# Kernel tuning notes

Hardware: AMD Instinct MI355X
Metric: run time of the kernel (lower is better)

Reference implementation:

```python
import jax, jax.numpy as jnp
import numpy as np
from jax import lax

B, N, C, H = 8, 1024, 384, 6
D = C // H
SCALE = D ** -0.5
EPS = 1e-5


def setup_inputs() -> dict:
    key = jax.random.key(0)
    ks = jax.random.split(key, 10)
    s = 0.02
    return {
        "x": jax.random.normal(ks[0], (B, N, C), jnp.float32),
        "w_qkv": jax.random.normal(ks[1], (3 * C, C), jnp.float32) * s,
        "w_proj": jax.random.normal(ks[2], (C, C), jnp.float32) * s,
        "b_proj": jax.random.normal(ks[3], (C,), jnp.float32) * s,
        "w_kq": jax.random.normal(ks[4], (H, 1, 3, 3), jnp.float32) * 0.1,   # depthwise (groups=H)
        "b_kq": jax.random.normal(ks[5], (H,), jnp.float32) * 0.1,
        "w_head": jax.random.normal(ks[6], (H, H, 1, 1), jnp.float32) * 0.1,  # 1x1 head-mixing conv
        "b_head": jax.random.normal(ks[7], (H,), jnp.float32) * 0.1,
        "gn_w": jnp.ones((H,), jnp.float32),
        "gn_b": jnp.zeros((H,), jnp.float32),
    }


def reference(x, w_qkv, w_proj, b_proj, w_kq, b_kq, w_head, b_head, gn_w, gn_b):
    # qkv projection (torch Linear: y = x @ W.T)
    qkv = (x @ w_qkv.T).reshape(B, N, 3, H, D).transpose(2, 0, 3, 1, 4)  # [3,B,H,N,D]
    q, k, v = qkv[0], qkv[1], qkv[2]

    # attention logits [B,H,N,N]
    logits = jnp.einsum("bhnd,bhmd->bhnm", q, k) * SCALE

    # depthwise (groups=H) 3x3 conv over the NxN logit map
    logits = lax.conv_general_dilated(
        logits, w_kq, window_strides=(1, 1), padding=((1, 1), (1, 1)),
        dimension_numbers=("NCHW", "OIHW", "NCHW"), feature_group_count=H,
    ) + b_kq[None, :, None, None]

    attn = jax.nn.softmax(logits, axis=-1)

    # 1x1 conv mixing heads
    attn = jnp.einsum("oh,bhnm->bonm", w_head[:, :, 0, 0], attn) + b_head[None, :, None, None]

    # GroupNorm(num_groups=H, channels=H): per (b, head) stats over NxN
    mean = attn.mean(axis=(2, 3), keepdims=True)
    var = ((attn - mean) ** 2).mean(axis=(2, 3), keepdims=True)
    attn = (attn - mean) * lax.rsqrt(var + EPS)
    attn = attn * gn_w[None, :, None, None] + gn_b[None, :, None, None]

    out = jnp.einsum("bhnm,bhmd->bhnd", attn, v)
    out = out.transpose(0, 2, 1, 3).reshape(B, N, C)
    return out @ w_proj.T + b_proj
```

## Files before the change

### kernel.cpp

```cpp
#include <hip/hip_runtime.h>

typedef unsigned short u16;
typedef __attribute__((ext_vector_type(8))) short short8;
typedef __attribute__((ext_vector_type(4))) float f32x4;

#define MFMA(a, b, c) __builtin_amdgcn_mfma_f32_16x16x32_bf16((a), (b), (c), 0, 0, 0)

__device__ inline float bf2f(u16 u) {
  union { unsigned int i; float f; } w; w.i = ((unsigned int)u) << 16; return w.f;
}
__device__ inline u16 f2bf(float x) {
  union { float f; unsigned int i; } u; u.f = x;
  unsigned int r = u.i + 0x7fffu + ((u.i >> 16) & 1u);
  return (u16)(r >> 16);
}
__device__ inline unsigned int pk2(float a, float b) {
  return (unsigned int)f2bf(a) | ((unsigned int)f2bf(b) << 16);
}
__device__ inline void unpack8(uint4 v, float* f) {
  union { unsigned int i; float g; } c;
  c.i = v.x << 16;          f[0] = c.g;
  c.i = v.x & 0xffff0000u;  f[1] = c.g;
  c.i = v.y << 16;          f[2] = c.g;
  c.i = v.y & 0xffff0000u;  f[3] = c.g;
  c.i = v.z << 16;          f[4] = c.g;
  c.i = v.z & 0xffff0000u;  f[5] = c.g;
  c.i = v.w << 16;          f[6] = c.g;
  c.i = v.w & 0xffff0000u;  f[7] = c.g;
}

static const size_t SZ_QKV = (size_t)48 * 1024 * 64 * 2;
static const size_t SZ_MAP = (size_t)48 * 1024 * 1024 * 2;
static const size_t OFF_Q  = 0;
static const size_t OFF_K  = OFF_Q + SZ_QKV;
static const size_t OFF_VT = OFF_K + SZ_QKV;
static const size_t OFF_S  = OFF_VT + SZ_QKV;
static const size_t OFF_U0 = OFF_S;
static const size_t OFF_U1 = OFF_S + 12582912;
static const size_t OFF_QM = OFF_S + SZ_MAP;
static const size_t OFF_OT = OFF_QM + SZ_MAP;
static const size_t OFF_ST = OFF_OT + SZ_QKV;
static const size_t OFF_CS = OFF_ST + 896;
static const size_t OFF_AD = OFF_CS + 12288;
static const size_t OFF_AL = OFF_AD + 12288;

__global__ __launch_bounds__(256) void k_qkv(const float* __restrict__ x,
                                             const float* __restrict__ w,
                                             u16* __restrict__ qb,
                                             u16* __restrict__ kb,
                                             u16* __restrict__ vT) {
  __shared__ u16 As[128 * 64];
  __shared__ u16 Bs[128 * 64];
  const int t = threadIdx.x;
  const int m0 = blockIdx.x * 128;
  const int n0 = blockIdx.y * 128;
  const int wave = t >> 6, lane = t & 63;
  const int wm = (wave & 1) * 64, wn = (wave >> 1) * 64;
  const int fr = lane & 15;
  const int fk = (lane >> 4) * 8;
  f32x4 acc[4][4] = {};
  for (int k0 = 0; k0 < 384; k0 += 64) {
#pragma unroll
    for (int i = 0; i < 4; ++i) {
      int e = (i * 256 + t) * 8;
      int row = e >> 6, col = e & 63;
      const float* xp = &x[(size_t)(m0 + row) * 384 + k0 + col];
      const float* wp = &w[(size_t)(n0 + row) * 384 + k0 + col];
      float4 a0 = *(const float4*)xp, a1 = *(const float4*)(xp + 4);
      uint4 av; av.x = pk2(a0.x, a0.y); av.y = pk2(a0.z, a0.w);
      av.z = pk2(a1.x, a1.y); av.w = pk2(a1.z, a1.w);
      *(uint4*)&As[e] = av;
      float4 b0 = *(const float4*)wp, b1 = *(const float4*)(wp + 4);
      uint4 bv; bv.x = pk2(b0.x, b0.y); bv.y = pk2(b0.z, b0.w);
      bv.z = pk2(b1.x, b1.y); bv.w = pk2(b1.z, b1.w);
      *(uint4*)&Bs[e] = bv;
    }
    __syncthreads();
#pragma unroll
    for (int ks = 0; ks < 2; ++ks) {
      const int ko = ks * 32 + fk;
      short8 a[4], b[4];
#pragma unroll
      for (int mi = 0; mi < 4; ++mi) a[mi] = *(const short8*)&As[(wm + mi * 16 + fr) * 64 + ko];
#pragma unroll
      for (int ni = 0; ni < 4; ++ni) b[ni] = *(const short8*)&Bs[(wn + ni * 16 + fr) * 64 + ko];
#pragma unroll
      for (int mi = 0; mi < 4; ++mi)
#pragma unroll
        for (int ni = 0; ni < 4; ++ni) acc[mi][ni] = MFMA(a[mi], b[ni], acc[mi][ni]);
    }
    __syncthreads();
  }
#pragma unroll
  for (int mi = 0; mi < 4; ++mi) {
#pragma unroll
    for (int ni = 0; ni < 4; ++ni) {
      int gc = n0 + wn + ni * 16 + fr;
      int s = gc / 384;
      int rem = gc - s * 384;
      int h = rem >> 6, d = rem & 63;
#pragma unroll
      for (int r = 0; r < 4; ++r) {
        int gm = m0 + wm + mi * 16 + (lane >> 4) * 4 + r;
        int b_ = gm >> 10, n = gm & 1023;
        u16 val = f2bf(acc[mi][ni][r]);
        size_t base = (size_t)(b_ * 6 + h) << 16;
        if (s == 0)      qb[base + (size_t)n * 64 + d] = val;
        else if (s == 1) kb[base + (size_t)n * 64 + d] = val;
        else             vT[base + (size_t)d * 1024 + n] = val;
      }
    }
  }
}

__global__ __launch_bounds__(256) void k_qk(const u16* __restrict__ qb,
                                            const u16* __restrict__ kb,
                                            u16* __restrict__ S) {
  __shared__ u16 As[128 * 64];
  __shared__ u16 Bs[128 * 64];
  const int t = threadIdx.x;
  const int m0 = blockIdx.x * 128, n0 = blockIdx.y * 128;
  const int bh = blockIdx.z;
  const u16* A = qb + ((size_t)bh << 16);
  const u16* Bp = kb + ((size_t)bh << 16);
  const int wave = t >> 6, lane = t & 63;
  const int wm = (wave & 1) * 64, wn = (wave >> 1) * 64;
  const int fr = lane & 15;
  const int fk = (lane >> 4) * 8;
  f32x4 acc[4][4] = {};
#pragma unroll
  for (int i = 0; i < 4; ++i) {
    int e = (i * 256 + t) * 8;
    *(uint4*)&As[e] = *(const uint4*)&A[(size_t)m0 * 64 + e];
    *(uint4*)&Bs[e] = *(const uint4*)&Bp[(size_t)n0 * 64 + e];
  }
  __syncthreads();
#pragma unroll
  for (int ks = 0; ks < 2; ++ks) {
    const int ko = ks * 32 + fk;
    short8 a[4], b[4];
#pragma unroll
    for (int mi = 0; mi < 4; ++mi) a[mi] = *(const short8*)&As[(wm + mi * 16 + fr) * 64 + ko];
#pragma unroll
    for (int ni = 0; ni < 4; ++ni) b[ni] = *(const short8*)&Bs[(wn + ni * 16 + fr) * 64 + ko];
#pragma unroll
    for (int mi = 0; mi < 4; ++mi)
#pragma unroll
      for (int ni = 0; ni < 4; ++ni) acc[mi][ni] = MFMA(a[mi], b[ni], acc[mi][ni]);
  }
  const size_t sb = (size_t)bh << 20;
#pragma unroll
  for (int mi = 0; mi < 4; ++mi)
#pragma unroll
    for (int ni = 0; ni < 4; ++ni) {
      int gc = n0 + wn + ni * 16 + fr;
#pragma unroll
      for (int r = 0; r < 4; ++r) {
        int gm = m0 + wm + mi * 16 + (lane >> 4) * 4 + r;
        S[sb + (size_t)gm * 1024 + gc] = f2bf(acc[mi][ni][r] * 0.125f);
      }
    }
}

__global__ __launch_bounds__(256) void k_conv_softmax(const u16* __restrict__ S,
                                                      const float* __restrict__ w_kq,
                                                      u16* __restrict__ Qb) {
  __shared__ u16 Sr[10 * 1040];
  __shared__ float red[4];
  const int t = threadIdx.x;
  const int bh = blockIdx.y;
  const int h = bh % 6;
  const int r0 = blockIdx.x * 8;
  const u16* Sp = S + ((size_t)bh << 20);
  float wv[9];
#pragma unroll
  for (int i = 0; i < 9; ++i) wv[i] = w_kq[h * 9 + i];
  if (t < 10) { Sr[t * 1040 + 7] = 0; Sr[t * 1040 + 1032] = 0; }
#pragma unroll
  for (int c = 0; c < 5; ++c) {
    int e = (c * 256 + t) * 8;
    int i = e >> 10, col = e & 1023;
    int g = r0 - 1 + i;
    uint4 val = make_uint4(0u, 0u, 0u, 0u);
    if (g >= 0 && g < 1024) val = *(const uint4*)&Sp[(size_t)g * 1024 + col];
    *(uint4*)&Sr[i * 1040 + 8 + col] = val;
  }
  __syncthreads();
  const int half = t >> 7;
  const int lane = t & 63;
  const int m0 = (t & 127) * 8;
  for (int pass = 0; pass < 4; ++pass) {
    int rr = pass * 2 + half;
    float o8[8];
#pragma unroll
    for (int j = 0; j < 8; ++j) o8[j] = 0.f;
#pragma unroll
    for (int i = 0; i < 3; ++i) {
      const u16* rowp = &Sr[(rr + i) * 1040 + 8];
      float left = bf2f(rowp[m0 - 1]);
      float md[8];
      unpack8(*(const uint4*)&rowp[m0], md);
      float right = bf2f(rowp[m0 + 8]);
      float w0 = wv[i * 3 + 0], w1 = wv[i * 3 + 1], w2 = wv[i * 3 + 2];
      o8[0] += w0 * left + w1 * md[0] + w2 * md[1];
#pragma unroll
      for (int j = 1; j < 7; ++j) o8[j] += w0 * md[j - 1] + w1 * md[j] + w2 * md[j + 1];
      o8[7] += w0 * md[6] + w1 * md[7] + w2 * right;
    }
    float mx = o8[0];
#pragma unroll
    for (int j = 1; j < 8; ++j) mx = fmaxf(mx, o8[j]);
    for (int off = 32; off; off >>= 1) mx = fmaxf(mx, __shfl_xor(mx, off, 64));
    if (lane == 0) red[t >> 6] = mx;
    __syncthreads();
    float rmax = fmaxf(red[half * 2], red[half * 2 + 1]);
    __syncthreads();
    float e8[8], s = 0.f;
#pragma unroll
    for (int j = 0; j < 8; ++j) { e8[j] = __expf(o8[j] - rmax); s += e8[j]; }
    for (int off = 32; off; off >>= 1) s += __shfl_xor(s, off, 64);
    if (lane == 0) red[t >> 6] = s;
    __syncthreads();
    float rsum = red[half * 2] + red[half * 2 + 1];
    __syncthreads();
    float scale = 1024.f / rsum;
    unsigned int pk[4];
#pragma unroll
    for (int jj = 0; jj < 4; ++jj)
      pk[jj] = pk2(e8[2 * jj] * scale - 1.f, e8[2 * jj + 1] * scale - 1.f);
    int n = r0 + rr;
    *(uint4*)&Qb[((size_t)bh << 20) + (size_t)n * 1024 + m0] = make_uint4(pk[0], pk[1], pk[2], pk[3]);
  }
}

__global__ __launch_bounds__(256) void k_colsum(const u16* __restrict__ vT,
                                                float* __restrict__ colsum) {
  __shared__ float acc[64];
  const int t = threadIdx.x;
  const int bh = blockIdx.x;
  if (t < 64) acc[t] = 0.f;
  __syncthreads();
  const int lane = t & 63;
  for (int c = 0; c < 32; ++c) {
    size_t l = (size_t)c * 2048 + (size_t)t * 8;
    uint4 u = *(const uint4*)&vT[((size_t)bh << 16) + l];
    float f[8];
    unpack8(u, f);
    float part = f[0] + f[1] + f[2] + f[3] + f[4] + f[5] + f[6] + f[7];
    for (int off = 32; off; off >>= 1) part += __shfl_xor(part, off, 64);
    if (lane == 0) atomicAdd(&acc[(int)(l >> 10)], part);
  }
  __syncthreads();
  if (t < 64) colsum[bh * 64 + t] = acc[t];
}

__global__ __launch_bounds__(256) void k_pvmix(const u16* __restrict__ Qm,
                                               const u16* __restrict__ vT,
                                               const float* __restrict__ wh,
                                               float* __restrict__ U0,
                                               float* __restrict__ U1,
                                               float* __restrict__ stats) {
  __shared__ u16 Am[64 * 72];
  __shared__ u16 Vm[64 * 72];
  const int t = threadIdx.x;
  const int n0 = blockIdx.x * 64;
  const int bo = blockIdx.y;
  const int mh = blockIdx.z;
  const int b_ = bo / 6, o = bo - b_ * 6;
  const int wave = t >> 6, lane = t & 63;
  const int fr = lane & 15, quad = lane >> 4;
  const int srow = t >> 3, smg8 = (t & 7) * 8;
  float wo[6];
#pragma unroll
  for (int hh = 0; hh < 6; ++hh) wo[hh] = wh[o * 6 + hh];
  const size_t qbase = ((size_t)(b_ * 6)) << 20;
  const u16* vp = vT + ((size_t)bo << 16);
  const int mstart = mh * 512;
  uint4 qpre[2][6];
  uint4 vpre[2];
  {
    const int m = mstart + smg8;
#pragma unroll
    for (int i = 0; i < 2; ++i)
#pragma unroll
      for (int hh = 0; hh < 6; ++hh)
        qpre[i][hh] = *(const uint4*)&Qm[qbase + (((size_t)hh) << 20) +
                                         (size_t)(n0 + i * 32 + srow) * 1024 + m];
    vpre[0] = *(const uint4*)&vp[(size_t)srow * 1024 + m];
    vpre[1] = *(const uint4*)&vp[(size_t)(32 + srow) * 1024 + m];
  }
  f32x4 acc[4] = {};
  float s1 = 0.f, s2 = 0.f;
  for (int mc = 0; mc < 8; ++mc) {
    __syncthreads();
#pragma unroll
    for (int i = 0; i < 2; ++i) {
      float mix[8] = {0.f, 0.f, 0.f, 0.f, 0.f, 0.f, 0.f, 0.f};
#pragma unroll
      for (int hh = 0; hh < 6; ++hh) {
        float qf[8];
        unpack8(qpre[i][hh], qf);
        float w = wo[hh];
#pragma unroll
        for (int j = 0; j < 8; ++j) mix[j] += w * qf[j];
      }
#pragma unroll
      for (int j = 0; j < 8; ++j) { s1 += mix[j]; s2 += mix[j] * mix[j]; }
      uint4 pk4;
      pk4.x = pk2(mix[0], mix[1]); pk4.y = pk2(mix[2], mix[3]);
      pk4.z = pk2(mix[4], mix[5]); pk4.w = pk2(mix[6], mix[7]);
      *(uint4*)&Am[(i * 32 + srow) * 72 + smg8] = pk4;
    }
    *(uint4*)&Vm[srow * 72 + smg8] = vpre[0];
    *(uint4*)&Vm[(32 + srow) * 72 + smg8] = vpre[1];
    if (mc < 7) {
      const int m = mstart + (mc + 1) * 64 + smg8;
#pragma unroll
      for (int i = 0; i < 2; ++i)
#pragma unroll
        for (int hh = 0; hh < 6; ++hh)
          qpre[i][hh] = *(const uint4*)&Qm[qbase + (((size_t)hh) << 20) +
                                           (size_t)(n0 + i * 32 + srow) * 1024 + m];
      vpre[0] = *(const uint4*)&vp[(size_t)srow * 1024 + m];
      vpre[1] = *(const uint4*)&vp[(size_t)(32 + srow) * 1024 + m];
    }
    __syncthreads();
#pragma unroll
    for (int ks = 0; ks < 2; ++ks) {
      short8 a = *(const short8*)&Am[(wave * 16 + fr) * 72 + ks * 32 + quad * 8];
#pragma unroll
      for (int ni = 0; ni < 4; ++ni) {
        short8 b = *(const short8*)&Vm[(ni * 16 + fr) * 72 + ks * 32 + quad * 8];
        acc[ni] = MFMA(a, b, acc[ni]);
      }
    }
  }
  float* Up = mh ? U1 : U0;
#pragma unroll
  for (int ni = 0; ni < 4; ++ni) {
    int d = ni * 16 + fr;
#pragma unroll
    for (int r = 0; r < 4; ++r) {
      int n = n0 + wave * 16 + quad * 4 + r;
      Up[((size_t)(bo * 1024 + n)) * 64 + d] = acc[ni][r];
    }
  }
  for (int off = 32; off; off >>= 1) {
    s1 += __shfl_xor(s1, off, 64);
    s2 += __shfl_xor(s2, off, 64);
  }
  if (lane == 0) {
    atomicAdd(&stats[bo * 2 + 0], s1);
    atomicAdd(&stats[bo * 2 + 1], s2);
  }
}

__global__ __launch_bounds__(256) void k_finalize(const float* __restrict__ stats,
                                                  const float* __restrict__ colsum,
                                                  const float* __restrict__ gn_w,
                                                  const float* __restrict__ gn_b,
                                                  float* __restrict__ addend,
                                                  float* __restrict__ alphaArr) {
  int gid = blockIdx.x * 256 + threadIdx.x;
  int bo = gid >> 6, d = gid & 63;
  int o = bo % 6;
  float s1 = stats[bo * 2], s2 = stats[bo * 2 + 1];
  const float inv = 1.f / 1048576.f;
  float mu = s1 * inv;
  float var = s2 * inv - mu * mu;
  float alpha = gn_w[o] * rsqrtf(var + 1e-5f * 1048576.f);
  float beta = gn_b[o] - alpha * mu;
  addend[gid] = beta * colsum[gid];
  if (d == 0) alphaArr[bo] = alpha;
}

__global__ __launch_bounds__(256) void k_apply(const float* __restrict__ U0,
                                               const float* __restrict__ U1,
                                               const float* __restrict__ alphaArr,
                                               const float* __restrict__ addend,
                                               u16* __restrict__ otmp) {
  int i = blockIdx.x * 256 + threadIdx.x;
  int e = i * 4;
  int d4 = e & 63;
  int n = (e >> 6) & 1023;
  int bo = e >> 16;
  float al = alphaArr[bo];
  const float* ap = &addend[bo * 64 + d4];
  float4 u0 = *(const float4*)&U0[e];
  float4 u1 = *(const float4*)&U1[e];
  int b = bo / 6, o = bo - b * 6;
  uint2 w;
  w.x = pk2(al * (u0.x + u1.x) + ap[0], al * (u0.y + u1.y) + ap[1]);
  w.y = pk2(al * (u0.z + u1.z) + ap[2], al * (u0.w + u1.w) + ap[3]);
  *(uint2*)&otmp[((size_t)(b * 1024 + n)) * 384 + o * 64 + d4] = w;
}

__global__ __launch_bounds__(256) void k_proj(const u16* __restrict__ A,
                                              const float* __restrict__ w,
                                              const float* __restrict__ bias,
                                              float* __restrict__ out) {
  __shared__ u16 As[128 * 64];
  __shared__ u16 Bs[128 * 64];
  const int t = threadIdx.x;
  const int m0 = blockIdx.x * 128;
  const int n0 = blockIdx.y * 128;
  const int wave = t >> 6, lane = t & 63;
  const int wm = (wave & 1) * 64, wn = (wave >> 1) * 64;
  const int fr = lane & 15;
  const int fk = (lane >> 4) * 8;
  f32x4 acc[4][4] = {};
  for (int k0 = 0; k0 < 384; k0 += 64) {
#pragma unroll
    for (int i = 0; i < 4; ++i) {
      int e = (i * 256 + t) * 8;
      int row = e >> 6, col = e & 63;
      *(uint4*)&As[e] = *(const uint4*)&A[(size_t)(m0 + row) * 384 + k0 + col];
      const float* wp = &w[(size_t)(n0 + row) * 384 + k0 + col];
      float4 b0 = *(const float4*)wp, b1 = *(const float4*)(wp + 4);
      uint4 bv; bv.x = pk2(b0.x, b0.y); bv.y = pk2(b0.z, b0.w);
      bv.z = pk2(b1.x, b1.y); bv.w = pk2(b1.z, b1.w);
      *(uint4*)&Bs[e] = bv;
    }
    __syncthreads();
#pragma unroll
    for (int ks = 0; ks < 2; ++ks) {
      const int ko = ks * 32 + fk;
      short8 a[4], b[4];
#pragma unroll
      for (int mi = 0; mi < 4; ++mi) a[mi] = *(const short8*)&As[(wm + mi * 16 + fr) * 64 + ko];
#pragma unroll
      for (int ni = 0; ni < 4; ++ni) b[ni] = *(const short8*)&Bs[(wn + ni * 16 + fr) * 64 + ko];
#pragma unroll
      for (int mi = 0; mi < 4; ++mi)
#pragma unroll
        for (int ni = 0; ni < 4; ++ni) acc[mi][ni] = MFMA(a[mi], b[ni], acc[mi][ni]);
    }
    __syncthreads();
  }
#pragma unroll
  for (int mi = 0; mi < 4; ++mi)
#pragma unroll
    for (int ni = 0; ni < 4; ++ni) {
      int gc = n0 + wn + ni * 16 + fr;
      float bv = bias[gc];
#pragma unroll
      for (int r = 0; r < 4; ++r) {
        int gm = m0 + wm + mi * 16 + (lane >> 4) * 4 + r;
        out[(size_t)gm * 384 + gc] = acc[mi][ni][r] + bv;
      }
    }
}

extern "C" void kernel_launch(void* const* d_in, const int* in_sizes, int n_in,
                              void* d_out, int out_size, void* d_ws, size_t ws_size,
                              hipStream_t stream) {
  (void)in_sizes; (void)n_in; (void)out_size; (void)ws_size;
  const float* x      = (const float*)d_in[0];
  const float* w_qkv  = (const float*)d_in[1];
  const float* w_proj = (const float*)d_in[2];
  const float* b_proj = (const float*)d_in[3];
  const float* w_kq   = (const float*)d_in[4];
  const float* w_head = (const float*)d_in[6];
  const float* gn_w   = (const float*)d_in[8];
  const float* gn_b   = (const float*)d_in[9];

  char* ws = (char*)d_ws;
  u16*   qb      = (u16*)(ws + OFF_Q);
  u16*   kb      = (u16*)(ws + OFF_K);
  u16*   vT      = (u16*)(ws + OFF_VT);
  u16*   Sb      = (u16*)(ws + OFF_S);
  float* U0      = (float*)(ws + OFF_U0);
  float* U1      = (float*)(ws + OFF_U1);
  u16*   Qm      = (u16*)(ws + OFF_QM);
  u16*   otmp    = (u16*)(ws + OFF_OT);
  float* stats   = (float*)(ws + OFF_ST);
  float* colsum  = (float*)(ws + OFF_CS);
  float* addend  = (float*)(ws + OFF_AD);
  float* alphaA  = (float*)(ws + OFF_AL);

  hipMemsetAsync(stats, 0, 512, stream);
  k_qkv<<<dim3(64, 9), 256, 0, stream>>>(x, w_qkv, qb, kb, vT);
  k_qk<<<dim3(8, 8, 48), 256, 0, stream>>>(qb, kb, Sb);
  k_conv_softmax<<<dim3(128, 48), 256, 0, stream>>>(Sb, w_kq, Qm);
  k_colsum<<<dim3(48), 256, 0, stream>>>(vT, colsum);
  k_pvmix<<<dim3(16, 48, 2), 256, 0, stream>>>(Qm, vT, w_head, U0, U1, stats);
  k_finalize<<<dim3(12), 256, 0, stream>>>(stats, colsum, gn_w, gn_b, addend, alphaA);
  k_apply<<<dim3(3072), 256, 0, stream>>>(U0, U1, alphaA, addend, otmp);
  k_proj<<<dim3(64, 3), 256, 0, stream>>>(otmp, w_proj, b_proj, (float*)d_out);
}
```

Measured before the change: 316.1 us.

## Compute two output heads per pvmix block and fuse GroupNorm apply into proj

k_pvmix now handles two mixed output heads per block. The six bf16 Qm head tiles are loaded and unpacked once and reused for both outputs, so Qm global reads are cut by half. Waves are re-split across output head and d-half, with each wave holding 4x2 MFMA accumulators. k_apply and its bf16 otmp buffer are removed, and k_proj now reads U0/U1 directly, applying alpha and the addend during its A-tile load. The trade-off is that k_proj redoes this apply work for each of its three column blocks and reads fp32 partials with strided addressing.

```diff
diff --git a/kernel.cpp b/kernel.cpp
--- a/kernel.cpp
+++ b/kernel.cpp
@@ -38,8 +38,7 @@
 static const size_t OFF_U0 = OFF_S;
 static const size_t OFF_U1 = OFF_S + 12582912;
 static const size_t OFF_QM = OFF_S + SZ_MAP;
-static const size_t OFF_OT = OFF_QM + SZ_MAP;
-static const size_t OFF_ST = OFF_OT + SZ_QKV;
+static const size_t OFF_ST = OFF_QM + SZ_MAP;
 static const size_t OFF_CS = OFF_ST + 896;
 static const size_t OFF_AD = OFF_CS + 12288;
 static const size_t OFF_AL = OFF_AD + 12288;
@@ -260,24 +259,30 @@
                                                float* __restrict__ U0,
                                                float* __restrict__ U1,
                                                float* __restrict__ stats) {
-  __shared__ u16 Am[64 * 72];
-  __shared__ u16 Vm[64 * 72];
+  __shared__ u16 Am[2][64 * 72];
+  __shared__ u16 Vm[2][64 * 72];
   const int t = threadIdx.x;
-  const int n0 = blockIdx.x * 64;
-  const int bo = blockIdx.y;
-  const int mh = blockIdx.z;
-  const int b_ = bo / 6, o = bo - b_ * 6;
+  const int n0 = (blockIdx.x >> 1) * 64;
+  const int mh = blockIdx.x & 1;
+  const int b_ = blockIdx.y;
+  const int o0 = blockIdx.z * 2;
+  const int bo0 = b_ * 6 + o0;
   const int wave = t >> 6, lane = t & 63;
   const int fr = lane & 15, quad = lane >> 4;
+  const int ow = wave >> 1;
+  const int dh = wave & 1;
   const int srow = t >> 3, smg8 = (t & 7) * 8;
-  float wo[6];
-#pragma unroll
-  for (int hh = 0; hh < 6; ++hh) wo[hh] = wh[o * 6 + hh];
+  float wo[2][6];
+#pragma unroll
+  for (int oi = 0; oi < 2; ++oi)
+#pragma unroll
+    for (int hh = 0; hh < 6; ++hh) wo[oi][hh] = wh[(o0 + oi) * 6 + hh];
   const size_t qbase = ((size_t)(b_ * 6)) << 20;
-  const u16* vp = vT + ((size_t)bo << 16);
+  const u16* vp0 = vT + ((size_t)bo0 << 16);
+  const u16* vp1 = vT + ((size_t)(bo0 + 1) << 16);
   const int mstart = mh * 512;
   uint4 qpre[2][6];
-  uint4 vpre[2];
+  uint4 vpre[2][2];
   {
     const int m = mstart + smg8;
 #pragma unroll
@@ -286,33 +291,41 @@
       for (int hh = 0; hh < 6; ++hh)
         qpre[i][hh] = *(const uint4*)&Qm[qbase + (((size_t)hh) << 20) +
                                          (size_t)(n0 + i * 32 + srow) * 1024 + m];
-    vpre[0] = *(const uint4*)&vp[(size_t)srow * 1024 + m];
-    vpre[1] = *(const uint4*)&vp[(size_t)(32 + srow) * 1024 + m];
-  }
-  f32x4 acc[4] = {};
-  float s1 = 0.f, s2 = 0.f;
+    vpre[0][0] = *(const uint4*)&vp0[(size_t)srow * 1024 + m];
+    vpre[0][1] = *(const uint4*)&vp0[(size_t)(32 + srow) * 1024 + m];
+    vpre[1][0] = *(const uint4*)&vp1[(size_t)srow * 1024 + m];
+    vpre[1][1] = *(const uint4*)&vp1[(size_t)(32 + srow) * 1024 + m];
+  }
+  f32x4 acc[4][2] = {};
+  float s1[2] = {0.f, 0.f}, s2[2] = {0.f, 0.f};
   for (int mc = 0; mc < 8; ++mc) {
     __syncthreads();
 #pragma unroll
     for (int i = 0; i < 2; ++i) {
-      float mix[8] = {0.f, 0.f, 0.f, 0.f, 0.f, 0.f, 0.f, 0.f};
-#pragma unroll
-      for (int hh = 0; hh < 6; ++hh) {
-        float qf[8];
-        unpack8(qpre[i][hh], qf);
-        float w = wo[hh];
-#pragma unroll
-        for (int j = 0; j < 8; ++j) mix[j] += w * qf[j];
+      float qf[6][8];
+#pragma unroll
+      for (int hh = 0; hh < 6; ++hh) unpack8(qpre[i][hh], qf[hh]);
+#pragma unroll
+      for (int oi = 0; oi < 2; ++oi) {
+        float mix[8] = {0.f, 0.f, 0.f, 0.f, 0.f, 0.f, 0.f, 0.f};
+#pragma unroll
+        for (int hh = 0; hh < 6; ++hh) {
+          float w = wo[oi][hh];
+#pragma unroll
+          for (int j = 0; j < 8; ++j) mix[j] += w * qf[hh][j];
+        }
+#pragma unroll
+        for (int j = 0; j < 8; ++j) { s1[oi] += mix[j]; s2[oi] += mix[j] * mix[j]; }
+        uint4 pk4;
+        pk4.x = pk2(mix[0], mix[1]); pk4.y = pk2(mix[2], mix[3]);
+        pk4.z = pk2(mix[4], mix[5]); pk4.w = pk2(mix[6], mix[7]);
+        *(uint4*)&Am[oi][(i * 32 + srow) * 72 + smg8] = pk4;
       }
-#pragma unroll
-      for (int j = 0; j < 8; ++j) { s1 += mix[j]; s2 += mix[j] * mix[j]; }
-      uint4 pk4;
-      pk4.x = pk2(mix[0], mix[1]); pk4.y = pk2(mix[2], mix[3]);
-      pk4.z = pk2(mix[4], mix[5]); pk4.w = pk2(mix[6], mix[7]);
-      *(uint4*)&Am[(i * 32 + srow) * 72 + smg8] = pk4;
-    }
-    *(uint4*)&Vm[srow * 72 + smg8] = vpre[0];
-    *(uint4*)&Vm[(32 + srow) * 72 + smg8] = vpre[1];
+    }
+    *(uint4*)&Vm[0][srow * 72 + smg8] = vpre[0][0];
+    *(uint4*)&Vm[0][(32 + srow) * 72 + smg8] = vpre[0][1];
+    *(uint4*)&Vm[1][srow * 72 + smg8] = vpre[1][0];
+    *(uint4*)&Vm[1][(32 + srow) * 72 + smg8] = vpre[1][1];
     if (mc < 7) {
       const int m = mstart + (mc + 1) * 64 + smg8;
 #pragma unroll
@@ -321,37 +334,50 @@
         for (int hh = 0; hh < 6; ++hh)
           qpre[i][hh] = *(const uint4*)&Qm[qbase + (((size_t)hh) << 20) +
                                            (size_t)(n0 + i * 32 + srow) * 1024 + m];
-      vpre[0] = *(const uint4*)&vp[(size_t)srow * 1024 + m];
-      vpre[1] = *(const uint4*)&vp[(size_t)(32 + srow) * 1024 + m];
+      vpre[0][0] = *(const uint4*)&vp0[(size_t)srow * 1024 + m];
+      vpre[0][1] = *(const uint4*)&vp0[(size_t)(32 + srow) * 1024 + m];
+      vpre[1][0] = *(const uint4*)&vp1[(size_t)srow * 1024 + m];
+      vpre[1][1] = *(const uint4*)&vp1[(size_t)(32 + srow) * 1024 + m];
     }
     __syncthreads();
 #pragma unroll
     for (int ks = 0; ks < 2; ++ks) {
-      short8 a = *(const short8*)&Am[(wave * 16 + fr) * 72 + ks * 32 + quad * 8];
-#pragma unroll
-      for (int ni = 0; ni < 4; ++ni) {
-        short8 b = *(const short8*)&Vm[(ni * 16 + fr) * 72 + ks * 32 + quad * 8];
-        acc[ni] = MFMA(a, b, acc[ni]);
+      short8 a[4];
+#pragma unroll
+      for (int nt = 0; nt < 4; ++nt)
+        a[nt] = *(const short8*)&Am[ow][(nt * 16 + fr) * 72 + ks * 32 + quad * 8];
+#pragma unroll
+      for (int ni = 0; ni < 2; ++ni) {
+        short8 b = *(const short8*)&Vm[ow][(dh * 32 + ni * 16 + fr) * 72 + ks * 32 + quad * 8];
+#pragma unroll
+        for (int nt = 0; nt < 4; ++nt) acc[nt][ni] = MFMA(a[nt], b, acc[nt][ni]);
       }
     }
   }
   float* Up = mh ? U1 : U0;
-#pragma unroll
-  for (int ni = 0; ni < 4; ++ni) {
-    int d = ni * 16 + fr;
-#pragma unroll
-    for (int r = 0; r < 4; ++r) {
-      int n = n0 + wave * 16 + quad * 4 + r;
-      Up[((size_t)(bo * 1024 + n)) * 64 + d] = acc[ni][r];
-    }
-  }
-  for (int off = 32; off; off >>= 1) {
-    s1 += __shfl_xor(s1, off, 64);
-    s2 += __shfl_xor(s2, off, 64);
-  }
-  if (lane == 0) {
-    atomicAdd(&stats[bo * 2 + 0], s1);
-    atomicAdd(&stats[bo * 2 + 1], s2);
+  const int bo = bo0 + ow;
+#pragma unroll
+  for (int nt = 0; nt < 4; ++nt)
+#pragma unroll
+    for (int ni = 0; ni < 2; ++ni) {
+      int d = dh * 32 + ni * 16 + fr;
+#pragma unroll
+      for (int r = 0; r < 4; ++r) {
+        int n = n0 + nt * 16 + quad * 4 + r;
+        Up[((size_t)(bo * 1024 + n)) * 64 + d] = acc[nt][ni][r];
+      }
+    }
+#pragma unroll
+  for (int oi = 0; oi < 2; ++oi) {
+    float a = s1[oi], q = s2[oi];
+    for (int off = 32; off; off >>= 1) {
+      a += __shfl_xor(a, off, 64);
+      q += __shfl_xor(q, off, 64);
+    }
+    if (lane == 0) {
+      atomicAdd(&stats[(bo0 + oi) * 2 + 0], a);
+      atomicAdd(&stats[(bo0 + oi) * 2 + 1], q);
+    }
   }
 }
 
@@ -374,28 +400,10 @@
   if (d == 0) alphaArr[bo] = alpha;
 }
 
-__global__ __launch_bounds__(256) void k_apply(const float* __restrict__ U0,
-                                               const float* __restrict__ U1,
-                                               const float* __restrict__ alphaArr,
-                                               const float* __restrict__ addend,
-                                               u16* __restrict__ otmp) {
-  int i = blockIdx.x * 256 + threadIdx.x;
-  int e = i * 4;
-  int d4 = e & 63;
-  int n = (e >> 6) & 1023;
-  int bo = e >> 16;
-  float al = alphaArr[bo];
-  const float* ap = &addend[bo * 64 + d4];
-  float4 u0 = *(const float4*)&U0[e];
-  float4 u1 = *(const float4*)&U1[e];
-  int b = bo / 6, o = bo - b * 6;
-  uint2 w;
-  w.x = pk2(al * (u0.x + u1.x) + ap[0], al * (u0.y + u1.y) + ap[1]);
-  w.y = pk2(al * (u0.z + u1.z) + ap[2], al * (u0.w + u1.w) + ap[3]);
-  *(uint2*)&otmp[((size_t)(b * 1024 + n)) * 384 + o * 64 + d4] = w;
-}
-
-__global__ __launch_bounds__(256) void k_proj(const u16* __restrict__ A,
+__global__ __launch_bounds__(256) void k_proj(const float* __restrict__ U0,
+                                              const float* __restrict__ U1,
+                                              const float* __restrict__ alphaArr,
+                                              const float* __restrict__ addend,
                                               const float* __restrict__ w,
                                               const float* __restrict__ bias,
                                               float* __restrict__ out) {
@@ -414,7 +422,22 @@
     for (int i = 0; i < 4; ++i) {
       int e = (i * 256 + t) * 8;
       int row = e >> 6, col = e & 63;
-      *(uint4*)&As[e] = *(const uint4*)&A[(size_t)(m0 + row) * 384 + k0 + col];
+      int gm = m0 + row;
+      int b_ = gm >> 10, n = gm & 1023;
+      int c = k0 + col;
+      int o = c >> 6, d0 = c & 63;
+      int bo = b_ * 6 + o;
+      size_t ue = ((size_t)(bo * 1024 + n)) * 64 + d0;
+      float4 u0a = *(const float4*)&U0[ue], u0b = *(const float4*)&U0[ue + 4];
+      float4 u1a = *(const float4*)&U1[ue], u1b = *(const float4*)&U1[ue + 4];
+      float al = alphaArr[bo];
+      const float* ap = &addend[bo * 64 + d0];
+      uint4 av;
+      av.x = pk2(al * (u0a.x + u1a.x) + ap[0], al * (u0a.y + u1a.y) + ap[1]);
+      av.y = pk2(al * (u0a.z + u1a.z) + ap[2], al * (u0a.w + u1a.w) + ap[3]);
+      av.z = pk2(al * (u0b.x + u1b.x) + ap[4], al * (u0b.y + u1b.y) + ap[5]);
+      av.w = pk2(al * (u0b.z + u1b.z) + ap[6], al * (u0b.w + u1b.w) + ap[7]);
+      *(uint4*)&As[e] = av;
       const float* wp = &w[(size_t)(n0 + row) * 384 + k0 + col];
       float4 b0 = *(const float4*)wp, b1 = *(const float4*)(wp + 4);
       uint4 bv; bv.x = pk2(b0.x, b0.y); bv.y = pk2(b0.z, b0.w);
@@ -472,7 +495,6 @@
   float* U0      = (float*)(ws + OFF_U0);
   float* U1      = (float*)(ws + OFF_U1);
   u16*   Qm      = (u16*)(ws + OFF_QM);
-  u16*   otmp    = (u16*)(ws + OFF_OT);
   float* stats   = (float*)(ws + OFF_ST);
   float* colsum  = (float*)(ws + OFF_CS);
   float* addend  = (float*)(ws + OFF_AD);
@@ -483,8 +505,7 @@
   k_qk<<<dim3(8, 8, 48), 256, 0, stream>>>(qb, kb, Sb);
   k_conv_softmax<<<dim3(128, 48), 256, 0, stream>>>(Sb, w_kq, Qm);
   k_colsum<<<dim3(48), 256, 0, stream>>>(vT, colsum);
-  k_pvmix<<<dim3(16, 48, 2), 256, 0, stream>>>(Qm, vT, w_head, U0, U1, stats);
+  k_pvmix<<<dim3(32, 8, 3), 256, 0, stream>>>(Qm, vT, w_head, U0, U1, stats);
   k_finalize<<<dim3(12), 256, 0, stream>>>(stats, colsum, gn_w, gn_b, addend, alphaA);
-  k_apply<<<dim3(3072), 256, 0, stream>>>(U0, U1, alphaA, addend, otmp);
-  k_proj<<<dim3(64, 3), 256, 0, stream>>>(otmp, w_proj, b_proj, (float*)d_out);
-}
+  k_proj<<<dim3(64, 3), 256, 0, stream>>>(U0, U1, alphaA, addend, w_proj, b_proj, (float*)d_out);
+}
```

New measurement: 324.6 us. 1.03x slower.
